# Performance work log

Measured on AMD Instinct MI355X. Metric: run time of the kernel, lower is better.

## Reference

```python
import jax, jax.numpy as jnp
import numpy as np

B, N, H = 32, 256, 1024
HEADS, NHID = 8, 128
NCLS = 7
BAND = 24
ALPHA = 0.2          # GAT leaky-relu slope
NEG = -9e15          # masked-attention fill, as in pyGAT


def setup_inputs() -> dict:
    key = jax.random.key(0)
    ks = jax.random.split(key, 16)
    def nrm(k, shp, s=0.02):
        return jax.random.normal(k, shp, dtype=jnp.float32) * s
    hidden_cls = jax.random.normal(ks[0], (B, N, H), dtype=jnp.float32)
    hidden_emo = jax.random.normal(ks[1], (B, N, H), dtype=jnp.float32)
    # causal band cliques, diagonal included (GAT uses clique - eye)
    t = jnp.arange(N)
    band = ((t[None, :] <= t[:, None]) & (t[None, :] > t[:, None] - BAND)).astype(jnp.float32)
    clique = jnp.broadcast_to(band, (B, N, N))
    labels = jax.random.randint(ks[2], (B, N), 0, NCLS)
    pooler_W = nrm(ks[3], (H, H)); pooler_b = jnp.zeros((H,), jnp.float32)
    gat_W = nrm(ks[4], (HEADS, H, NHID))
    gat_a1 = nrm(ks[5], (HEADS, NHID)); gat_a2 = nrm(ks[6], (HEADS, NHID))
    out_W = nrm(ks[7], (H, H))            # heads*nhid == H -> nclass=H
    out_a1 = nrm(ks[8], (H,)); out_a2 = nrm(ks[9], (H,))
    lin1_W = nrm(ks[10], (H, H)); lin1_b = jnp.zeros((H,), jnp.float32)
    lin0_W = nrm(ks[11], (2 * H, H)); lin0_b = jnp.zeros((H,), jnp.float32)
    cls_W = nrm(ks[12], (H, NCLS)); cls_b = jnp.zeros((NCLS,), jnp.float32)
    A = jax.random.uniform(ks[13], (NCLS, NCLS), dtype=jnp.float32) + 0.1
    hmm_A = A / A.sum(axis=1, keepdims=True)   # row-stochastic transition matrix
    return dict(hidden_cls=hidden_cls, hidden_emo=hidden_emo, clique=clique,
                labels=labels, pooler_W=pooler_W, pooler_b=pooler_b,
                gat_W=gat_W, gat_a1=gat_a1, gat_a2=gat_a2,
                out_W=out_W, out_a1=out_a1, out_a2=out_a2,
                lin1_W=lin1_W, lin1_b=lin1_b, lin0_W=lin0_W, lin0_b=lin0_b,
                cls_W=cls_W, cls_b=cls_b, hmm_A=hmm_A)


def _lrelu(x):
    return jnp.where(x > 0, x, ALPHA * x)


def reference(hidden_cls, hidden_emo, clique, labels, pooler_W, pooler_b,
              gat_W, gat_a1, gat_a2, out_W, out_a1, out_a2,
              lin1_W, lin1_b, lin0_W, lin0_b, cls_W, cls_b, hmm_A):
    # PoolerAll: dense + tanh on all token states (dropout = identity in eval)
    fea_cls = jnp.tanh(hidden_cls @ pooler_W + pooler_b)   # [B,N,H] (CLS per utt)
    fea_emo = jnp.tanh(hidden_emo @ pooler_W + pooler_b)   # [B,N,H] (mask tok per utt)

    eyeN = jnp.eye(N, dtype=clique.dtype)
    adjm = (clique - eyeN) > 0                             # [B,N,N] GAT adjacency

    def gat_one(x, am):                                    # x [N,H], am [N,N]
        Wh = jnp.einsum('nf,hfd->hnd', x, gat_W)           # [heads,N,nhid]
        e = _lrelu(jnp.einsum('hnd,hd->hn', Wh, gat_a1)[:, :, None]
                   + jnp.einsum('hnd,hd->hn', Wh, gat_a2)[:, None, :])
        att = jax.nn.softmax(jnp.where(am[None], e, NEG), axis=-1)
        h1 = jax.nn.elu(jnp.einsum('hnm,hmd->hnd', att, Wh))
        h1 = jnp.transpose(h1, (1, 0, 2)).reshape(N, HEADS * NHID)
        Wh2 = h1 @ out_W                                   # out attention layer (concat=False)
        e2 = _lrelu((Wh2 @ out_a1)[:, None] + (Wh2 @ out_a2)[None, :])
        h2 = jax.nn.softmax(jnp.where(am, e2, NEG), axis=-1) @ Wh2
        return jax.nn.elu(h2)                              # [N,H]

    gat_out = jax.vmap(gat_one)(fea_cls, adjm)             # [B,N,H]
    # row 0 replaced by (dropout of) fea_cls row 0, as in the original
    g = jnp.concatenate([fea_cls[:, :1], gat_out[:, 1:]], axis=1)
    g = jnp.concatenate([fea_cls, g @ lin1_W + lin1_b], axis=-1) @ lin0_W + lin0_b
    log_gat = jax.nn.softmax(g @ cls_W + cls_b, axis=-1)   # [B,N,NCLS] (probs)

    # HMM emission probs hmm_B(fea) = softmax(classifier(fea))
    Bprob = jax.nn.softmax(fea_emo @ cls_W + cls_b, axis=-1)  # [B,N,NCLS]
    P0 = jnp.full((NCLS,), 1.0 / NCLS, dtype=jnp.float32)
    AT = hmm_A.T

    def hmm_row(Bp, mrow):                                 # Bp [N,NCLS], mrow [N]
        def step(carry, xs):
            p, started = carry
            bt, m = xs
            p_init = P0 * bt; p_init = p_init / p_init.sum()
            p_tr = (AT @ p) * bt; p_tr = p_tr / p_tr.sum()
            p_new = jnp.where(started, p_tr, p_init)
            valid = m > 0.5
            return (jnp.where(valid, p_new, p), started | valid), None
        (p, _), _ = jax.lax.scan(step, (P0, jnp.asarray(False)), (Bp, mrow))
        return p                                           # final filtered posterior

    log_hmm = jax.vmap(lambda Bp, M: jax.vmap(lambda mr: hmm_row(Bp, mr))(M))(Bprob, clique)

    logits = jnp.log((log_gat + log_hmm) * 0.5).reshape(B * N, NCLS)
    lab = labels.reshape(B * N)
    mask = lab >= 0
    picked = jnp.take_along_axis(logits, jnp.where(mask, lab, 0)[:, None], axis=1)[:, 0]
    loss = -(jnp.where(mask, picked, 0.0).sum() / jnp.maximum(mask.sum(), 1).astype(jnp.float32))
    return loss, logits
```

## Files before the change

### kernel.cpp

```cpp
#include <hip/hip_runtime.h>
#include <hip/hip_bf16.h>
#include <math.h>

typedef __hip_bfloat16 bf16;
typedef __attribute__((ext_vector_type(8))) short short8;
typedef __attribute__((ext_vector_type(4))) float float4v;

static constexpr int Bb = 32, Nn = 256, Hh = 1024, HEADS = 8, NHID = 128, NCLS = 7, BAND = 24;
static constexpr int M = Bb * Nn;
static constexpr float ALPHA = 0.2f;
static constexpr long INEL = (long)M * Hh;

__device__ __forceinline__ float tof(bf16 x) { return __bfloat162float(x); }
__device__ __forceinline__ bf16 tob(float x) { return __float2bfloat16(x); }
__device__ __forceinline__ unsigned short f2bits(float x) {
    bf16 h = __float2bfloat16(x);
    return *(unsigned short*)&h;
}
__device__ __forceinline__ float bits2f(unsigned short u) {
    unsigned v = ((unsigned)u) << 16;
    float f;
    __builtin_memcpy(&f, &v, 4);
    return f;
}

__device__ __forceinline__ void gload16(const void* g, void* l) {
    __builtin_amdgcn_global_load_lds(
        (const __attribute__((address_space(1))) void*)g,
        (__attribute__((address_space(3))) void*)l, 16, 0, 0);
}

static constexpr long OFF_PWT  = 0;
static constexpr long OFF_PB   = 1048576;
static constexpr long OFF_WCT  = 1049600;
static constexpr long OFF_GA1  = 2098176;
static constexpr long OFF_GA2  = 2099200;
static constexpr long OFF_OWT  = 2100224;
static constexpr long OFF_OA1  = 3148800;
static constexpr long OFF_OA2  = 3149824;
static constexpr long OFF_L1WT = 3150848;
static constexpr long OFF_L1B  = 4199424;
static constexpr long OFF_L0WT = 4200448;
static constexpr long OFF_L0B  = 6297600;
static constexpr long OFF_CWT  = 6298624;
static constexpr long OFF_CB   = 6305792;
static constexpr long OFF_HA   = 6305799;
static constexpr long W_TOTAL  = 6305848;

__global__ void probe_k(const void* __restrict__ p, int* __restrict__ flag) {
    int t = threadIdx.x;
    int bad = 0;
    for (int i = t; i < 4096; i += 256) {
        float v = tof(((const bf16*)p)[i]);
        if (!(fabsf(v) < 1e4f)) bad = 1;
    }
    __shared__ int sb[256];
    sb[t] = bad; __syncthreads();
    for (int s = 128; s; s >>= 1) { if (t < s) sb[t] |= sb[t + s]; __syncthreads(); }
    if (t == 0) *flag = sb[0] ? 0 : 1;
}

__device__ __forceinline__ float ldany(const void* p, long i, int isb) {
    return isb ? tof(((const bf16*)p)[i]) : ((const float*)p)[i];
}

__global__ void convert_k(const int* __restrict__ flagp,
                          const void* pW, const void* pb, const void* gW,
                          const void* ga1, const void* ga2, const void* oW,
                          const void* oa1, const void* oa2, const void* l1W,
                          const void* l1b, const void* l0W, const void* l0b,
                          const void* cW, const void* cb, const void* hA,
                          bf16* __restrict__ dst) {
    long idx = (long)blockIdx.x * 256 + threadIdx.x;
    if (idx >= W_TOTAL) return;
    int isb = *flagp;
    const void* src; long si;
    if      (idx < OFF_PB)   { long l = idx;            long n = l >> 10, k = l & 1023;
                               src = pW;  si = k * 1024 + n; }
    else if (idx < OFF_WCT)  { src = pb;  si = idx - OFF_PB; }
    else if (idx < OFF_GA1)  { long l = idx - OFF_WCT;  long n = l >> 10, f = l & 1023;
                               long h = n >> 7, d = n & 127;
                               src = gW;  si = h * 131072 + f * 128 + d; }
    else if (idx < OFF_GA2)  { src = ga1; si = idx - OFF_GA1; }
    else if (idx < OFF_OWT)  { src = ga2; si = idx - OFF_GA2; }
    else if (idx < OFF_OA1)  { long l = idx - OFF_OWT;  long n = l >> 10, k = l & 1023;
                               src = oW;  si = k * 1024 + n; }
    else if (idx < OFF_OA2)  { src = oa1; si = idx - OFF_OA1; }
    else if (idx < OFF_L1WT) { src = oa2; si = idx - OFF_OA2; }
    else if (idx < OFF_L1B)  { long l = idx - OFF_L1WT; long n = l >> 10, k = l & 1023;
                               src = l1W; si = k * 1024 + n; }
    else if (idx < OFF_L0WT) { src = l1b; si = idx - OFF_L1B; }
    else if (idx < OFF_L0B)  { long l = idx - OFF_L0WT; long n = l >> 11, k = l & 2047;
                               src = l0W; si = k * 1024 + n; }
    else if (idx < OFF_CWT)  { src = l0b; si = idx - OFF_L0B; }
    else if (idx < OFF_CB)   { long l = idx - OFF_CWT;  long c = l >> 10, k = l & 1023;
                               src = cW;  si = k * 7 + c; }
    else if (idx < OFF_HA)   { src = cb;  si = idx - OFF_CB; }
    else                     { src = hA;  si = idx - OFF_HA; }
    dst[idx] = tob(ldany(src, si, isb));
}

__global__ void convin_k(const int* __restrict__ flagp, const void* __restrict__ s0,
                         const void* __restrict__ s1, bf16* __restrict__ d0,
                         bf16* __restrict__ d1) {
    const int isb = *flagp;
    long i = ((long)blockIdx.x * 256 + threadIdx.x) * 8;
    const void* s; bf16* d; long off;
    if (i < INEL) { s = s0; d = d0; off = i; }
    else          { s = s1; d = d1; off = i - INEL; }
    if (isb) {
        *(int4*)(d + off) = *(const int4*)((const bf16*)s + off);
    } else {
        const float* f = (const float*)s + off;
        unsigned short tmp[8];
        #pragma unroll
        for (int q = 0; q < 8; ++q) tmp[q] = f2bits(f[q]);
        *(int4*)(d + off) = *(int4*)tmp;
    }
}

template <int ACT>
__device__ __forceinline__ void gemm_core(const bf16* __restrict__ A,
                                          const bf16* __restrict__ Bt,
                                          const bf16* __restrict__ bias,
                                          bf16* __restrict__ Cout,
                                          unsigned short* As, unsigned short* Bs,
                                          int Nc, int K, int bm, int bn) {
    const int tid = threadIdx.x;
    const int lane = tid & 63;
    const int wave = tid >> 6;
    const int wm = (wave >> 1) * 64, wn = (wave & 1) * 64;
    const int l15 = lane & 15, quad = lane >> 4;
    const int r0 = wave * 32;
    const int lrow = lane >> 2, q = lane & 3;
    const int rA = r0 + lrow, rB = r0 + 16 + lrow;
    const int qa = (q ^ (rA & 3) ^ ((rA >> 2) & 3)) * 8;
    const int qb = (q ^ (rB & 3) ^ ((rB >> 2) & 3)) * 8;
    const int sc8 = (quad ^ (l15 & 3) ^ (l15 >> 2)) * 8;

    float4v acc[4][4];
    #pragma unroll
    for (int i = 0; i < 4; ++i)
        #pragma unroll
        for (int j = 0; j < 4; ++j) acc[i][j] = (float4v){0.f, 0.f, 0.f, 0.f};

    const bf16* ga0 = A + (long)(bm + rA) * K + qa;
    const bf16* ga1 = A + (long)(bm + rB) * K + qb;
    const bf16* gb0 = Bt + (long)(bn + rA) * K + qa;
    const bf16* gb1 = Bt + (long)(bn + rB) * K + qb;

    for (int k0 = 0; k0 < K; k0 += 64) {
        gload16(ga0 + k0,      As + r0 * 32);
        gload16(ga1 + k0,      As + (r0 + 16) * 32);
        gload16(ga0 + k0 + 32, As + 4096 + r0 * 32);
        gload16(ga1 + k0 + 32, As + 4096 + (r0 + 16) * 32);
        gload16(gb0 + k0,      Bs + r0 * 32);
        gload16(gb1 + k0,      Bs + (r0 + 16) * 32);
        gload16(gb0 + k0 + 32, Bs + 4096 + r0 * 32);
        gload16(gb1 + k0 + 32, Bs + 4096 + (r0 + 16) * 32);
        __syncthreads();
        #pragma unroll
        for (int ks = 0; ks < 2; ++ks) {
            const unsigned short* Au = As + ks * 4096;
            const unsigned short* Bu = Bs + ks * 4096;
            short8 af[4], bfr[4];
            #pragma unroll
            for (int i = 0; i < 4; ++i)
                af[i] = *(const short8*)(Au + (wm + i * 16 + l15) * 32 + sc8);
            #pragma unroll
            for (int j = 0; j < 4; ++j)
                bfr[j] = *(const short8*)(Bu + (wn + j * 16 + l15) * 32 + sc8);
            #pragma unroll
            for (int i = 0; i < 4; ++i)
                #pragma unroll
                for (int j = 0; j < 4; ++j)
                    acc[i][j] = __builtin_amdgcn_mfma_f32_16x16x32_bf16(af[i], bfr[j], acc[i][j], 0, 0, 0);
        }
        __syncthreads();
    }
    #pragma unroll
    for (int j = 0; j < 4; ++j) {
        int gn = bn + wn + j * 16 + l15;
        float bj = bias ? tof(bias[gn]) : 0.f;
        #pragma unroll
        for (int i = 0; i < 4; ++i) {
            #pragma unroll
            for (int r = 0; r < 4; ++r) {
                int gm = bm + wm + i * 16 + quad * 4 + r;
                float v = acc[i][j][r] + bj;
                if (ACT == 1) v = tanhf(v);
                Cout[(long)gm * Nc + gn] = tob(v);
            }
        }
    }
}

template <int ACT>
__global__ __launch_bounds__(256) void gemm_fast_k(const bf16* __restrict__ A,
                                                   const bf16* __restrict__ Bt,
                                                   const bf16* __restrict__ bias,
                                                   bf16* __restrict__ Cout,
                                                   int Nc, int K) {
    __shared__ unsigned short As[2 * 128 * 32];
    __shared__ unsigned short Bs[2 * 128 * 32];
    gemm_core<ACT>(A, Bt, bias, Cout, As, Bs, Nc, K, blockIdx.x * 128, blockIdx.y * 128);
}

__global__ __launch_bounds__(256) void gemmP_k(const bf16* __restrict__ A0,
                                               const bf16* __restrict__ A1,
                                               const bf16* __restrict__ Bt,
                                               const bf16* __restrict__ bias,
                                               bf16* __restrict__ C0,
                                               bf16* __restrict__ C1) {
    __shared__ unsigned short As[2 * 128 * 32];
    __shared__ unsigned short Bs[2 * 128 * 32];
    const bf16* A = blockIdx.z ? A1 : A0;
    bf16* C = blockIdx.z ? C1 : C0;
    gemm_core<1>(A, Bt, bias, C, As, Bs, Hh, Hh, blockIdx.x * 128, blockIdx.y * 128);
}

__global__ __launch_bounds__(256) void gemm2_fast_k(const bf16* __restrict__ A1,
                                                    const bf16* __restrict__ A2,
                                                    const bf16* __restrict__ Bt,
                                                    const bf16* __restrict__ bias,
                                                    bf16* __restrict__ Cout) {
    constexpr int Nc = 1024, K = 2048;
    __shared__ unsigned short As[2 * 128 * 32];
    __shared__ unsigned short Bs[2 * 128 * 32];
    const int tid = threadIdx.x;
    const int lane = tid & 63;
    const int wave = tid >> 6;
    const int wm = (wave >> 1) * 64, wn = (wave & 1) * 64;
    const int l15 = lane & 15, quad = lane >> 4;
    const int r0 = wave * 32;
    const int lrow = lane >> 2, q = lane & 3;
    const int rA = r0 + lrow, rB = r0 + 16 + lrow;
    const int qa = (q ^ (rA & 3) ^ ((rA >> 2) & 3)) * 8;
    const int qb = (q ^ (rB & 3) ^ ((rB >> 2) & 3)) * 8;
    const int sc8 = (quad ^ (l15 & 3) ^ (l15 >> 2)) * 8;
    const int bm = blockIdx.x * 128, bn = blockIdx.y * 128;

    float4v acc[4][4];
    #pragma unroll
    for (int i = 0; i < 4; ++i)
        #pragma unroll
        for (int j = 0; j < 4; ++j) acc[i][j] = (float4v){0.f, 0.f, 0.f, 0.f};

    const bf16* gb0 = Bt + (long)(bn + rA) * K + qa;
    const bf16* gb1 = Bt + (long)(bn + rB) * K + qb;
    for (int k0 = 0; k0 < K; k0 += 64) {
        const bf16* Asrc = (k0 < 1024) ? A1 : A2;
        int kl = k0 & 1023;
        const bf16* ga0 = Asrc + (long)(bm + rA) * 1024 + kl + qa;
        const bf16* ga1 = Asrc + (long)(bm + rB) * 1024 + kl + qb;
        gload16(ga0,      As + r0 * 32);
        gload16(ga1,      As + (r0 + 16) * 32);
        gload16(ga0 + 32, As + 4096 + r0 * 32);
        gload16(ga1 + 32, As + 4096 + (r0 + 16) * 32);
        gload16(gb0 + k0,      Bs + r0 * 32);
        gload16(gb1 + k0,      Bs + (r0 + 16) * 32);
        gload16(gb0 + k0 + 32, Bs + 4096 + r0 * 32);
        gload16(gb1 + k0 + 32, Bs + 4096 + (r0 + 16) * 32);
        __syncthreads();
        #pragma unroll
        for (int ks = 0; ks < 2; ++ks) {
            const unsigned short* Au = As + ks * 4096;
            const unsigned short* Bu = Bs + ks * 4096;
            short8 af[4], bfr[4];
            #pragma unroll
            for (int i = 0; i < 4; ++i)
                af[i] = *(const short8*)(Au + (wm + i * 16 + l15) * 32 + sc8);
            #pragma unroll
            for (int j = 0; j < 4; ++j)
                bfr[j] = *(const short8*)(Bu + (wn + j * 16 + l15) * 32 + sc8);
            #pragma unroll
            for (int i = 0; i < 4; ++i)
                #pragma unroll
                for (int j = 0; j < 4; ++j)
                    acc[i][j] = __builtin_amdgcn_mfma_f32_16x16x32_bf16(af[i], bfr[j], acc[i][j], 0, 0, 0);
        }
        __syncthreads();
    }
    #pragma unroll
    for (int j = 0; j < 4; ++j) {
        int gn = bn + wn + j * 16 + l15;
        float bj = tof(bias[gn]);
        #pragma unroll
        for (int i = 0; i < 4; ++i)
            #pragma unroll
            for (int r = 0; r < 4; ++r) {
                int gm = bm + wm + i * 16 + quad * 4 + r;
                Cout[(long)gm * Nc + gn] = tob(acc[i][j][r] + bj);
            }
    }
}

__global__ __launch_bounds__(256) void att1f_k(const bf16* __restrict__ Wh,
                                               const bf16* __restrict__ ga1,
                                               const bf16* __restrict__ ga2,
                                               bf16* __restrict__ h1) {
    __shared__ unsigned short S[152][128];
    __shared__ float f1s[152], f2s[152];
    __shared__ float att[128][25];
    const int bx = blockIdx.x;
    const int b = bx >> 4, h = (bx >> 1) & 7, half = bx & 1;
    const int nbase = half * 128;
    const int mstart = half ? (nbase - (BAND - 1)) : 0;
    const int mcount = half ? (256 - mstart) : 128;
    const int t = threadIdx.x;
    const int c = t & 15;

    float av1[8], av2[8];
    {
        union { int4 v; unsigned short us[8]; } u1, u2;
        u1.v = *(const int4*)(ga1 + h * 128 + c * 8);
        u2.v = *(const int4*)(ga2 + h * 128 + c * 8);
        #pragma unroll
        for (int qq = 0; qq < 8; ++qq) { av1[qq] = bits2f(u1.us[qq]); av2[qq] = bits2f(u2.us[qq]); }
    }

    const int iters = (mcount * 16 + 255) >> 8;
    for (int i = 0; i < iters; ++i) {
        int li = i * 256 + t;
        int mr = li >> 4;
        if (mr < mcount) {
            long ga = (long)(b * 256 + mstart + mr) * 1024 + h * 128 + c * 8;
            union { int4 v; unsigned short us[8]; } u;
            u.v = *(const int4*)(Wh + ga);
            float p1 = 0.f, p2 = 0.f;
            #pragma unroll
            for (int qq = 0; qq < 8; ++qq) {
                float f = bits2f(u.us[qq]);
                p1 += f * av1[qq]; p2 += f * av2[qq];
            }
            *(int4*)&S[mr][c * 8] = u.v;
            #pragma unroll
            for (int mask = 1; mask < 16; mask <<= 1) {
                p1 += __shfl_xor(p1, mask);
                p2 += __shfl_xor(p2, mask);
            }
            if (c == 0) { f1s[mr] = p1; f2s[mr] = p2; }
        }
    }
    __syncthreads();

    if (t < 128) {
        int n = nbase + t;
        if (n > 0) {
            int cnt = n < (BAND - 1) ? n : (BAND - 1);
            int m0 = n - cnt;
            float f1n = f1s[n - mstart];
            float e[BAND - 1];
            float mx = -1e30f;
            for (int i = 0; i < cnt; ++i) {
                float v = f1n + f2s[m0 + i - mstart];
                v = v > 0.f ? v : ALPHA * v;
                e[i] = v; mx = fmaxf(mx, v);
            }
            float ss = 0.f;
            for (int i = 0; i < cnt; ++i) { e[i] = __expf(e[i] - mx); ss += e[i]; }
            float inv = 1.0f / ss;
            for (int i = 0; i < cnt; ++i) att[t][i] = e[i] * inv;
        }
    }
    __syncthreads();

    const int wave = t >> 6, lane = t & 63;
    for (int ln = wave; ln < 128; ln += 4) {
        int n = nbase + ln;
        if (n == 0) continue;
        int cnt = n < (BAND - 1) ? n : (BAND - 1);
        int mr0 = n - cnt - mstart;
        float s0 = 0.f, s1 = 0.f;
        for (int i = 0; i < cnt; ++i) {
            float a = att[ln][i];
            unsigned u = *(const unsigned*)&S[mr0 + i][lane * 2];
            s0 += a * bits2f((unsigned short)(u & 0xffff));
            s1 += a * bits2f((unsigned short)(u >> 16));
        }
        s0 = s0 > 0.f ? s0 : expm1f(s0);
        s1 = s1 > 0.f ? s1 : expm1f(s1);
        unsigned out = (unsigned)f2bits(s0) | ((unsigned)f2bits(s1) << 16);
        *(unsigned*)(h1 + (long)(b * 256 + n) * 1024 + h * 128 + lane * 2) = out;
    }
}

__global__ void mean1_k(const bf16* __restrict__ Wh, bf16* __restrict__ h1) {
    int bh = blockIdx.x;
    int h = bh & 7, b = bh >> 3;
    int lane = threadIdx.x;
    float s0 = 0.f, s1 = 0.f;
    long base = (long)(b * 256) * 1024 + h * 128 + lane * 2;
    for (int m = 0; m < 256; ++m) {
        unsigned u = *(const unsigned*)(Wh + base + (long)m * 1024);
        s0 += bits2f((unsigned short)(u & 0xffff));
        s1 += bits2f((unsigned short)(u >> 16));
    }
    s0 *= (1.0f / 256.0f); s1 *= (1.0f / 256.0f);
    s0 = s0 > 0.f ? s0 : expm1f(s0);
    s1 = s1 > 0.f ? s1 : expm1f(s1);
    unsigned out = (unsigned)f2bits(s0) | ((unsigned)f2bits(s1) << 16);
    *(unsigned*)(h1 + base) = out;
}

__global__ void f12b_k(const bf16* __restrict__ Wh2, const bf16* __restrict__ a1,
                       const bf16* __restrict__ a2, float* __restrict__ f1b,
                       float* __restrict__ f2b) {
    int idx = blockIdx.x;
    int lane = threadIdx.x;
    const bf16* row = Wh2 + (long)idx * 1024 + lane * 16;
    float s1 = 0.f, s2 = 0.f;
    #pragma unroll
    for (int half = 0; half < 2; ++half) {
        union { int4 v; unsigned short us[8]; } x, w1, w2;
        x.v  = *(const int4*)(row + half * 8);
        w1.v = *(const int4*)(a1 + lane * 16 + half * 8);
        w2.v = *(const int4*)(a2 + lane * 16 + half * 8);
        #pragma unroll
        for (int q = 0; q < 8; ++q) {
            float f = bits2f(x.us[q]);
            s1 += f * bits2f(w1.us[q]);
            s2 += f * bits2f(w2.us[q]);
        }
    }
    #pragma unroll
    for (int off = 32; off; off >>= 1) {
        s1 += __shfl_down(s1, off);
        s2 += __shfl_down(s2, off);
    }
    if (lane == 0) { f1b[idx] = s1; f2b[idx] = s2; }
}

__global__ __launch_bounds__(256) void att2f_k(const bf16* __restrict__ Wh2,
                                               const float* __restrict__ f1b,
                                               const float* __restrict__ f2b,
                                               bf16* __restrict__ g) {
    __shared__ unsigned short S[152][128];
    __shared__ float att[128][25];
    const int bx = blockIdx.x;
    const int b = bx >> 4, half = (bx >> 3) & 1, jt = bx & 7;
    const int nbase = half * 128;
    const int mstart = half ? (nbase - (BAND - 1)) : 0;
    const int mcount = half ? (256 - mstart) : 128;
    const int t = threadIdx.x;
    const int c = t & 15;

    const int iters = (mcount * 16 + 255) >> 8;
    for (int i = 0; i < iters; ++i) {
        int li = i * 256 + t;
        int mr = li >> 4;
        if (mr < mcount) {
            long ga = (long)(b * 256 + mstart + mr) * 1024 + jt * 128 + c * 8;
            *(int4*)&S[mr][c * 8] = *(const int4*)(Wh2 + ga);
        }
    }
    __syncthreads();

    if (t < 128) {
        int n = nbase + t;
        if (n > 0) {
            int cnt = n < (BAND - 1) ? n : (BAND - 1);
            int m0 = n - cnt;
            float f1n = f1b[b * 256 + n];
            float e[BAND - 1];
            float mx = -1e30f;
            for (int i = 0; i < cnt; ++i) {
                float v = f1n + f2b[b * 256 + m0 + i];
                v = v > 0.f ? v : ALPHA * v;
                e[i] = v; mx = fmaxf(mx, v);
            }
            float ss = 0.f;
            for (int i = 0; i < cnt; ++i) { e[i] = __expf(e[i] - mx); ss += e[i]; }
            float inv = 1.0f / ss;
            for (int i = 0; i < cnt; ++i) att[t][i] = e[i] * inv;
        }
    }
    __syncthreads();

    const int wave = t >> 6, lane = t & 63;
    for (int ln = wave; ln < 128; ln += 4) {
        int n = nbase + ln;
        if (n == 0) continue;
        int cnt = n < (BAND - 1) ? n : (BAND - 1);
        int mr0 = n - cnt - mstart;
        float s0 = 0.f, s1 = 0.f;
        for (int i = 0; i < cnt; ++i) {
            float a = att[ln][i];
            unsigned u = *(const unsigned*)&S[mr0 + i][lane * 2];
            s0 += a * bits2f((unsigned short)(u & 0xffff));
            s1 += a * bits2f((unsigned short)(u >> 16));
        }
        s0 = s0 > 0.f ? s0 : expm1f(s0);
        s1 = s1 > 0.f ? s1 : expm1f(s1);
        unsigned out = (unsigned)f2bits(s0) | ((unsigned)f2bits(s1) << 16);
        *(unsigned*)(g + (long)(b * 256 + n) * 1024 + jt * 128 + lane * 2) = out;
    }
}

__global__ void g_row0_k(const bf16* __restrict__ fea_cls, bf16* __restrict__ g) {
    int b = blockIdx.x;
    int t = threadIdx.x;
    long base = (long)(b * 256) * 1024 + t * 8;
    *(int4*)(g + base) = *(const int4*)(fea_cls + base);
}

__global__ void cls7_k(const bf16* __restrict__ X, const bf16* __restrict__ Wt,
                       const bf16* __restrict__ b, float* __restrict__ out, int K) {
    int row = blockIdx.x;
    int lane = threadIdx.x;
    float xv[16];
    {
        const bf16* x = X + (long)row * K + lane * 16;
        union { int4 v; unsigned short us[8]; } u0, u1;
        u0.v = *(const int4*)x; u1.v = *(const int4*)(x + 8);
        #pragma unroll
        for (int q = 0; q < 8; ++q) { xv[q] = bits2f(u0.us[q]); xv[q + 8] = bits2f(u1.us[q]); }
    }
    float acc[NCLS];
    #pragma unroll
    for (int cc = 0; cc < NCLS; ++cc) {
        const bf16* wr = Wt + (long)cc * K + lane * 16;
        union { int4 v; unsigned short us[8]; } w0, w1;
        w0.v = *(const int4*)wr; w1.v = *(const int4*)(wr + 8);
        float s = 0.f;
        #pragma unroll
        for (int q = 0; q < 8; ++q) {
            s += xv[q] * bits2f(w0.us[q]);
            s += xv[q + 8] * bits2f(w1.us[q]);
        }
        acc[cc] = s;
    }
    #pragma unroll
    for (int cc = 0; cc < NCLS; ++cc)
        #pragma unroll
        for (int off = 32; off; off >>= 1) acc[cc] += __shfl_down(acc[cc], off);
    if (lane == 0) {
        float mx = -1e30f;
        #pragma unroll
        for (int cc = 0; cc < NCLS; ++cc) { acc[cc] += tof(b[cc]); mx = fmaxf(mx, acc[cc]); }
        float s = 0.f;
        #pragma unroll
        for (int cc = 0; cc < NCLS; ++cc) { acc[cc] = expf(acc[cc] - mx); s += acc[cc]; }
        float inv = 1.0f / s;
        #pragma unroll
        for (int cc = 0; cc < NCLS; ++cc) out[(long)row * NCLS + cc] = acc[cc] * inv;
    }
}

__global__ void hmm_k(const float* __restrict__ Bprob, const bf16* __restrict__ hmm_A,
                      float* __restrict__ out) {
    __shared__ float AT[NCLS][NCLS];
    int t = threadIdx.x;
    if (t < NCLS * NCLS) {
        int i = t / NCLS, j = t % NCLS;
        AT[i][j] = tof(hmm_A[j * NCLS + i]);
    }
    __syncthreads();
    int idx = blockIdx.x * blockDim.x + t;
    int n = idx & 255, b = idx >> 8;
    int t0 = n - (BAND - 1) > 0 ? n - (BAND - 1) : 0;
    const float* Bp = Bprob + (long)(b * 256) * NCLS;
    float p[NCLS];
    float s = 0.f;
    #pragma unroll
    for (int cc = 0; cc < NCLS; ++cc) { p[cc] = Bp[t0 * NCLS + cc]; s += p[cc]; }
    float inv = 1.0f / s;
    #pragma unroll
    for (int cc = 0; cc < NCLS; ++cc) p[cc] *= inv;
    for (int tt = t0 + 1; tt <= n; ++tt) {
        float q[NCLS]; float ss = 0.f;
        #pragma unroll
        for (int i = 0; i < NCLS; ++i) {
            float a = 0.f;
            #pragma unroll
            for (int j = 0; j < NCLS; ++j) a += AT[i][j] * p[j];
            a *= Bp[tt * NCLS + i];
            q[i] = a; ss += a;
        }
        float iv = 1.0f / ss;
        #pragma unroll
        for (int i = 0; i < NCLS; ++i) p[i] = q[i] * iv;
    }
    #pragma unroll
    for (int cc = 0; cc < NCLS; ++cc) out[(long)idx * NCLS + cc] = p[cc];
}

__global__ void zero_k(float* p) { *p = 0.f; }

__global__ void final_k(const float* __restrict__ lg, const float* __restrict__ lh,
                        const int* __restrict__ labels, void* __restrict__ out,
                        float* __restrict__ loss_acc, const int* __restrict__ flagp) {
    int idx = blockIdx.x * blockDim.x + threadIdx.x;
    const int isb = *flagp;
    float lo[NCLS];
    int lab = labels[idx];
    #pragma unroll
    for (int c = 0; c < NCLS; ++c) {
        float v = logf(0.5f * (lg[(long)idx * NCLS + c] + lh[(long)idx * NCLS + c]));
        lo[c] = v;
        long o = 1 + (long)idx * NCLS + c;
        if (isb) ((bf16*)out)[o] = tob(v);
        else     ((float*)out)[o] = v;
    }
    float picked = lo[lab];
    __shared__ float red[256];
    red[threadIdx.x] = picked;
    __syncthreads();
    for (int s = 128; s; s >>= 1) {
        if (threadIdx.x < s) red[threadIdx.x] += red[threadIdx.x + s];
        __syncthreads();
    }
    if (threadIdx.x == 0) atomicAdd(loss_acc, red[0]);
}

__global__ void loss_k(const float* __restrict__ acc, void* __restrict__ out,
                       const int* __restrict__ flagp) {
    float v = -acc[0] / (float)(Bb * Nn);
    if (*flagp) ((bf16*)out)[0] = tob(v);
    else        ((float*)out)[0] = v;
}

extern "C" void kernel_launch(void* const* d_in, const int* in_sizes, int n_in,
                              void* d_out, int out_size, void* d_ws, size_t ws_size,
                              hipStream_t stream) {
    const void* hidden_cls = d_in[0];
    const void* hidden_emo = d_in[1];
    const int* labels = (const int*)d_in[3];

    char* w = (char*)d_ws;
    bf16* C  = (bf16*)w;
    bf16* E  = C + INEL;
    bf16* Wb = E + INEL;
    bf16* H2 = Wb + INEL;
    bf16* wc = H2 + INEL;
    float* f1b   = (float*)(wc + W_TOTAL);
    float* f2b   = f1b + M;
    float* Bprob = f2b + M;
    float* lgat  = Bprob + (long)M * NCLS;
    float* lhmm  = lgat + (long)M * NCLS;
    float* loss_acc = lhmm + (long)M * NCLS;
    int*   flag  = (int*)(loss_acc + 1);

    dim3 gblk(256);
    dim3 ggrid(M / 128, Hh / 128);
    dim3 pgrid(M / 128, Hh / 128, 2);

    probe_k<<<1, 256, 0, stream>>>(d_in[4], flag);
    convert_k<<<(int)((W_TOTAL + 255) / 256), 256, 0, stream>>>(
        flag, d_in[4], d_in[5], d_in[6], d_in[7], d_in[8], d_in[9], d_in[10],
        d_in[11], d_in[12], d_in[13], d_in[14], d_in[15], d_in[16], d_in[17],
        d_in[18], wc);
    convin_k<<<(int)(2 * INEL / (256 * 8)), 256, 0, stream>>>(flag, hidden_emo, hidden_cls, Wb, H2);

    gemmP_k<<<pgrid, gblk, 0, stream>>>(Wb, H2, wc + OFF_PWT, wc + OFF_PB, E, C);
    cls7_k<<<M, 64, 0, stream>>>(E, wc + OFF_CWT, wc + OFF_CB, Bprob, Hh);
    gemm_fast_k<0><<<ggrid, gblk, 0, stream>>>(C, wc + OFF_WCT, (const bf16*)nullptr, Wb, Hh, Hh);
    att1f_k<<<512, 256, 0, stream>>>(Wb, wc + OFF_GA1, wc + OFF_GA2, E);
    mean1_k<<<Bb * HEADS, 64, 0, stream>>>(Wb, E);
    gemm_fast_k<0><<<ggrid, gblk, 0, stream>>>(E, wc + OFF_OWT, (const bf16*)nullptr, Wb, Hh, Hh);
    f12b_k<<<M, 64, 0, stream>>>(Wb, wc + OFF_OA1, wc + OFF_OA2, f1b, f2b);
    g_row0_k<<<Bb, 128, 0, stream>>>(C, E);
    att2f_k<<<512, 256, 0, stream>>>(Wb, f1b, f2b, E);
    gemm_fast_k<0><<<ggrid, gblk, 0, stream>>>(E, wc + OFF_L1WT, wc + OFF_L1B, Wb, Hh, Hh);
    gemm2_fast_k<<<ggrid, gblk, 0, stream>>>(C, Wb, wc + OFF_L0WT, wc + OFF_L0B, E);
    cls7_k<<<M, 64, 0, stream>>>(E, wc + OFF_CWT, wc + OFF_CB, lgat, Hh);
    hmm_k<<<M / 256, 256, 0, stream>>>(Bprob, wc + OFF_HA, lhmm);
    zero_k<<<1, 1, 0, stream>>>(loss_acc);
    final_k<<<M / 256, 256, 0, stream>>>(lgat, lhmm, labels, d_out, loss_acc, flag);
    loss_k<<<1, 1, 0, stream>>>(loss_acc, d_out, flag);
}
```

Measured before the change: 488.5 us.

## Fold lin1 GEMM into lin0 weights and fuse small kernels

Removes the separate lin1 GEMM over activations. The lin0 second-half weights are pre-multiplied with lin1_W inside the pooler GEMM launch (extra z-slice), and the folded bias is computed once in a small kernel. Conversion of weights and inputs is merged into one launch. The row-0 copy is folded into att2f, and the HMM filter is folded into the final loss kernel. This saves a full M×H×H GEMM and several launches, at the cost of an extra bf16 rounding of the combined weight product.

```diff
diff --git a/kernel.cpp b/kernel.cpp
--- a/kernel.cpp
+++ b/kernel.cpp
@@ -45,7 +45,9 @@
 static constexpr long OFF_CWT  = 6298624;
 static constexpr long OFF_CB   = 6305792;
 static constexpr long OFF_HA   = 6305799;
-static constexpr long W_TOTAL  = 6305848;
+static constexpr long OFF_L1WN = 6305848;
+static constexpr long W_TOTAL  = 7354424;
+static constexpr long CONV_TOTAL = W_TOTAL + (2 * INEL) / 8;
 
 __global__ void probe_k(const void* __restrict__ p, int* __restrict__ flag) {
     int t = threadIdx.x;
@@ -64,16 +66,34 @@
     return isb ? tof(((const bf16*)p)[i]) : ((const float*)p)[i];
 }
 
-__global__ void convert_k(const int* __restrict__ flagp,
+__global__ void convall_k(const int* __restrict__ flagp,
                           const void* pW, const void* pb, const void* gW,
                           const void* ga1, const void* ga2, const void* oW,
                           const void* oa1, const void* oa2, const void* l1W,
                           const void* l1b, const void* l0W, const void* l0b,
                           const void* cW, const void* cb, const void* hA,
-                          bf16* __restrict__ dst) {
+                          const void* in0, const void* in1,
+                          bf16* __restrict__ dst, bf16* __restrict__ din0,
+                          bf16* __restrict__ din1) {
     long idx = (long)blockIdx.x * 256 + threadIdx.x;
-    if (idx >= W_TOTAL) return;
+    if (idx >= CONV_TOTAL) return;
     int isb = *flagp;
+    if (idx >= W_TOTAL) {
+        long g = (idx - W_TOTAL) * 8;
+        const void* s; bf16* d; long off;
+        if (g < INEL) { s = in0; d = din0; off = g; }
+        else          { s = in1; d = din1; off = g - INEL; }
+        if (isb) {
+            *(int4*)(d + off) = *(const int4*)((const bf16*)s + off);
+        } else {
+            const float* f = (const float*)s + off;
+            unsigned short tmp[8];
+            #pragma unroll
+            for (int q = 0; q < 8; ++q) tmp[q] = f2bits(f[q]);
+            *(int4*)(d + off) = *(int4*)tmp;
+        }
+        return;
+    }
     const void* src; long si;
     if      (idx < OFF_PB)   { long l = idx;            long n = l >> 10, k = l & 1023;
                                src = pW;  si = k * 1024 + n; }
@@ -96,36 +116,29 @@
     else if (idx < OFF_CB)   { long l = idx - OFF_CWT;  long c = l >> 10, k = l & 1023;
                                src = cW;  si = k * 7 + c; }
     else if (idx < OFF_HA)   { src = cb;  si = idx - OFF_CB; }
-    else                     { src = hA;  si = idx - OFF_HA; }
+    else if (idx < OFF_L1WN) { src = hA;  si = idx - OFF_HA; }
+    else                     { src = l1W; si = idx - OFF_L1WN; }
     dst[idx] = tob(ldany(src, si, isb));
 }
 
-__global__ void convin_k(const int* __restrict__ flagp, const void* __restrict__ s0,
-                         const void* __restrict__ s1, bf16* __restrict__ d0,
-                         bf16* __restrict__ d1) {
-    const int isb = *flagp;
-    long i = ((long)blockIdx.x * 256 + threadIdx.x) * 8;
-    const void* s; bf16* d; long off;
-    if (i < INEL) { s = s0; d = d0; off = i; }
-    else          { s = s1; d = d1; off = i - INEL; }
-    if (isb) {
-        *(int4*)(d + off) = *(const int4*)((const bf16*)s + off);
-    } else {
-        const float* f = (const float*)s + off;
-        unsigned short tmp[8];
-        #pragma unroll
-        for (int q = 0; q < 8; ++q) tmp[q] = f2bits(f[q]);
-        *(int4*)(d + off) = *(int4*)tmp;
-    }
-}
-
-template <int ACT>
-__device__ __forceinline__ void gemm_core(const bf16* __restrict__ A,
-                                          const bf16* __restrict__ Bt,
+__global__ void bias2_k(const bf16* __restrict__ wc, bf16* __restrict__ b2) {
+    int n = blockIdx.x;
+    int lane = threadIdx.x;
+    const bf16* row = wc + OFF_L0WT + (long)n * 2048 + 1024;
+    const bf16* l1b = wc + OFF_L1B;
+    float s = 0.f;
+    for (int j = lane; j < 1024; j += 64) s += tof(l1b[j]) * tof(row[j]);
+    #pragma unroll
+    for (int off = 32; off; off >>= 1) s += __shfl_down(s, off);
+    if (lane == 0) b2[n] = tob(s + tof(wc[OFF_L0B + n]));
+}
+
+__device__ __forceinline__ void gemm_core(const bf16* __restrict__ A, int lda,
+                                          const bf16* __restrict__ Bt, int ldb,
                                           const bf16* __restrict__ bias,
                                           bf16* __restrict__ Cout,
                                           unsigned short* As, unsigned short* Bs,
-                                          int Nc, int K, int bm, int bn) {
+                                          int Nc, int K, int bm, int bn, int act) {
     const int tid = threadIdx.x;
     const int lane = tid & 63;
     const int wave = tid >> 6;
@@ -144,10 +157,10 @@
         #pragma unroll
         for (int j = 0; j < 4; ++j) acc[i][j] = (float4v){0.f, 0.f, 0.f, 0.f};
 
-    const bf16* ga0 = A + (long)(bm + rA) * K + qa;
-    const bf16* ga1 = A + (long)(bm + rB) * K + qb;
-    const bf16* gb0 = Bt + (long)(bn + rA) * K + qa;
-    const bf16* gb1 = Bt + (long)(bn + rB) * K + qb;
+    const bf16* ga0 = A + (long)(bm + rA) * lda + qa;
+    const bf16* ga1 = A + (long)(bm + rB) * lda + qb;
+    const bf16* gb0 = Bt + (long)(bn + rA) * ldb + qa;
+    const bf16* gb1 = Bt + (long)(bn + rB) * ldb + qb;
 
     for (int k0 = 0; k0 < K; k0 += 64) {
         gload16(ga0 + k0,      As + r0 * 32);
@@ -188,14 +201,13 @@
             for (int r = 0; r < 4; ++r) {
                 int gm = bm + wm + i * 16 + quad * 4 + r;
                 float v = acc[i][j][r] + bj;
-                if (ACT == 1) v = tanhf(v);
+                if (act == 1) v = tanhf(v);
                 Cout[(long)gm * Nc + gn] = tob(v);
             }
         }
     }
 }
 
-template <int ACT>
 __global__ __launch_bounds__(256) void gemm_fast_k(const bf16* __restrict__ A,
                                                    const bf16* __restrict__ Bt,
                                                    const bf16* __restrict__ bias,
@@ -203,7 +215,7 @@
                                                    int Nc, int K) {
     __shared__ unsigned short As[2 * 128 * 32];
     __shared__ unsigned short Bs[2 * 128 * 32];
-    gemm_core<ACT>(A, Bt, bias, Cout, As, Bs, Nc, K, blockIdx.x * 128, blockIdx.y * 128);
+    gemm_core(A, K, Bt, K, bias, Cout, As, Bs, Nc, K, blockIdx.x * 128, blockIdx.y * 128, 0);
 }
 
 __global__ __launch_bounds__(256) void gemmP_k(const bf16* __restrict__ A0,
@@ -211,20 +223,30 @@
                                                const bf16* __restrict__ Bt,
                                                const bf16* __restrict__ bias,
                                                bf16* __restrict__ C0,
-                                               bf16* __restrict__ C1) {
+                                               bf16* __restrict__ C1,
+                                               const bf16* __restrict__ wgA,
+                                               const bf16* __restrict__ wgB,
+                                               bf16* __restrict__ wgC) {
     __shared__ unsigned short As[2 * 128 * 32];
     __shared__ unsigned short Bs[2 * 128 * 32];
-    const bf16* A = blockIdx.z ? A1 : A0;
-    bf16* C = blockIdx.z ? C1 : C0;
-    gemm_core<1>(A, Bt, bias, C, As, Bs, Hh, Hh, blockIdx.x * 128, blockIdx.y * 128);
+    const int z = blockIdx.z;
+    if (z == 2) {
+        if (blockIdx.x >= 8) return;
+        gemm_core(wgA, 2048, wgB, 1024, (const bf16*)nullptr, wgC, As, Bs,
+                  1024, 1024, blockIdx.x * 128, blockIdx.y * 128, 0);
+    } else {
+        gemm_core(z ? A1 : A0, 1024, Bt, 1024, bias, z ? C1 : C0, As, Bs,
+                  1024, 1024, blockIdx.x * 128, blockIdx.y * 128, 1);
+    }
 }
 
 __global__ __launch_bounds__(256) void gemm2_fast_k(const bf16* __restrict__ A1,
+                                                    const bf16* __restrict__ B1,
                                                     const bf16* __restrict__ A2,
-                                                    const bf16* __restrict__ Bt,
+                                                    const bf16* __restrict__ B2,
                                                     const bf16* __restrict__ bias,
                                                     bf16* __restrict__ Cout) {
-    constexpr int Nc = 1024, K = 2048;
+    constexpr int Nc = 1024;
     __shared__ unsigned short As[2 * 128 * 32];
     __shared__ unsigned short Bs[2 * 128 * 32];
     const int tid = threadIdx.x;
@@ -246,21 +268,24 @@
         #pragma unroll
         for (int j = 0; j < 4; ++j) acc[i][j] = (float4v){0.f, 0.f, 0.f, 0.f};
 
-    const bf16* gb0 = Bt + (long)(bn + rA) * K + qa;
-    const bf16* gb1 = Bt + (long)(bn + rB) * K + qb;
-    for (int k0 = 0; k0 < K; k0 += 64) {
-        const bf16* Asrc = (k0 < 1024) ? A1 : A2;
-        int kl = k0 & 1023;
+    for (int k0 = 0; k0 < 2048; k0 += 64) {
+        const int sel = (k0 < 1024);
+        const bf16* Asrc = sel ? A1 : A2;
+        const bf16* Bsrc = sel ? B1 : B2;
+        const int ldb = sel ? 2048 : 1024;
+        const int kl = k0 & 1023;
         const bf16* ga0 = Asrc + (long)(bm + rA) * 1024 + kl + qa;
         const bf16* ga1 = Asrc + (long)(bm + rB) * 1024 + kl + qb;
+        const bf16* gb0 = Bsrc + (long)(bn + rA) * ldb + kl + qa;
+        const bf16* gb1 = Bsrc + (long)(bn + rB) * ldb + kl + qb;
         gload16(ga0,      As + r0 * 32);
         gload16(ga1,      As + (r0 + 16) * 32);
         gload16(ga0 + 32, As + 4096 + r0 * 32);
         gload16(ga1 + 32, As + 4096 + (r0 + 16) * 32);
-        gload16(gb0 + k0,      Bs + r0 * 32);
-        gload16(gb1 + k0,      Bs + (r0 + 16) * 32);
-        gload16(gb0 + k0 + 32, Bs + 4096 + r0 * 32);
-        gload16(gb1 + k0 + 32, Bs + 4096 + (r0 + 16) * 32);
+        gload16(gb0,      Bs + r0 * 32);
+        gload16(gb1,      Bs + (r0 + 16) * 32);
+        gload16(gb0 + 32, Bs + 4096 + r0 * 32);
+        gload16(gb1 + 32, Bs + 4096 + (r0 + 16) * 32);
         __syncthreads();
         #pragma unroll
         for (int ks = 0; ks < 2; ++ks) {
@@ -434,6 +459,7 @@
 __global__ __launch_bounds__(256) void att2f_k(const bf16* __restrict__ Wh2,
                                                const float* __restrict__ f1b,
                                                const float* __restrict__ f2b,
+                                               const bf16* __restrict__ fea_cls,
                                                bf16* __restrict__ g) {
     __shared__ unsigned short S[152][128];
     __shared__ float att[128][25];
@@ -444,6 +470,11 @@
     const int mcount = half ? (256 - mstart) : 128;
     const int t = threadIdx.x;
     const int c = t & 15;
+
+    if (half == 0 && t < 16) {
+        long base = (long)(b * 256) * 1024 + jt * 128 + t * 8;
+        *(int4*)(g + base) = *(const int4*)(fea_cls + base);
+    }
 
     const int iters = (mcount * 16 + 255) >> 8;
     for (int i = 0; i < iters; ++i) {
@@ -497,13 +528,6 @@
     }
 }
 
-__global__ void g_row0_k(const bf16* __restrict__ fea_cls, bf16* __restrict__ g) {
-    int b = blockIdx.x;
-    int t = threadIdx.x;
-    long base = (long)(b * 256) * 1024 + t * 8;
-    *(int4*)(g + base) = *(const int4*)(fea_cls + base);
-}
-
 __global__ void cls7_k(const bf16* __restrict__ X, const bf16* __restrict__ Wt,
                        const bf16* __restrict__ b, float* __restrict__ out, int K) {
     int row = blockIdx.x;
@@ -547,56 +571,49 @@
     }
 }
 
-__global__ void hmm_k(const float* __restrict__ Bprob, const bf16* __restrict__ hmm_A,
-                      float* __restrict__ out) {
+__global__ void zero_k(float* p) { *p = 0.f; }
+
+__global__ void final_k(const float* __restrict__ lg, const float* __restrict__ Bprob,
+                        const bf16* __restrict__ hmm_A, const int* __restrict__ labels,
+                        void* __restrict__ out, float* __restrict__ loss_acc,
+                        const int* __restrict__ flagp) {
     __shared__ float AT[NCLS][NCLS];
     int t = threadIdx.x;
-    if (t < NCLS * NCLS) {
-        int i = t / NCLS, j = t % NCLS;
-        AT[i][j] = tof(hmm_A[j * NCLS + i]);
-    }
+    if (t < NCLS * NCLS) AT[t / NCLS][t % NCLS] = tof(hmm_A[(t % NCLS) * NCLS + t / NCLS]);
     __syncthreads();
-    int idx = blockIdx.x * blockDim.x + t;
+    int idx = blockIdx.x * 256 + t;
     int n = idx & 255, b = idx >> 8;
     int t0 = n - (BAND - 1) > 0 ? n - (BAND - 1) : 0;
     const float* Bp = Bprob + (long)(b * 256) * NCLS;
     float p[NCLS];
-    float s = 0.f;
-    #pragma unroll
-    for (int cc = 0; cc < NCLS; ++cc) { p[cc] = Bp[t0 * NCLS + cc]; s += p[cc]; }
-    float inv = 1.0f / s;
-    #pragma unroll
-    for (int cc = 0; cc < NCLS; ++cc) p[cc] *= inv;
-    for (int tt = t0 + 1; tt <= n; ++tt) {
-        float q[NCLS]; float ss = 0.f;
-        #pragma unroll
-        for (int i = 0; i < NCLS; ++i) {
-            float a = 0.f;
-            #pragma unroll
-            for (int j = 0; j < NCLS; ++j) a += AT[i][j] * p[j];
-            a *= Bp[tt * NCLS + i];
-            q[i] = a; ss += a;
-        }
-        float iv = 1.0f / ss;
-        #pragma unroll
-        for (int i = 0; i < NCLS; ++i) p[i] = q[i] * iv;
-    }
-    #pragma unroll
-    for (int cc = 0; cc < NCLS; ++cc) out[(long)idx * NCLS + cc] = p[cc];
-}
-
-__global__ void zero_k(float* p) { *p = 0.f; }
-
-__global__ void final_k(const float* __restrict__ lg, const float* __restrict__ lh,
-                        const int* __restrict__ labels, void* __restrict__ out,
-                        float* __restrict__ loss_acc, const int* __restrict__ flagp) {
-    int idx = blockIdx.x * blockDim.x + threadIdx.x;
+    {
+        float s = 0.f;
+        #pragma unroll
+        for (int cc = 0; cc < NCLS; ++cc) { p[cc] = Bp[t0 * NCLS + cc]; s += p[cc]; }
+        float inv = 1.0f / s;
+        #pragma unroll
+        for (int cc = 0; cc < NCLS; ++cc) p[cc] *= inv;
+        for (int tt = t0 + 1; tt <= n; ++tt) {
+            float qv[NCLS]; float ss = 0.f;
+            #pragma unroll
+            for (int i = 0; i < NCLS; ++i) {
+                float a = 0.f;
+                #pragma unroll
+                for (int j = 0; j < NCLS; ++j) a += AT[i][j] * p[j];
+                a *= Bp[tt * NCLS + i];
+                qv[i] = a; ss += a;
+            }
+            float iv = 1.0f / ss;
+            #pragma unroll
+            for (int i = 0; i < NCLS; ++i) p[i] = qv[i] * iv;
+        }
+    }
     const int isb = *flagp;
+    int lab = labels[idx];
     float lo[NCLS];
-    int lab = labels[idx];
     #pragma unroll
     for (int c = 0; c < NCLS; ++c) {
-        float v = logf(0.5f * (lg[(long)idx * NCLS + c] + lh[(long)idx * NCLS + c]));
+        float v = logf(0.5f * (lg[(long)idx * NCLS + c] + p[c]));
         lo[c] = v;
         long o = 1 + (long)idx * NCLS + c;
         if (isb) ((bf16*)out)[o] = tob(v);
@@ -604,13 +621,13 @@
     }
     float picked = lo[lab];
     __shared__ float red[256];
-    red[threadIdx.x] = picked;
+    red[t] = picked;
     __syncthreads();
     for (int s = 128; s; s >>= 1) {
-        if (threadIdx.x < s) red[threadIdx.x] += red[threadIdx.x + s];
+        if (t < s) red[t] += red[t + s];
         __syncthreads();
     }
-    if (threadIdx.x == 0) atomicAdd(loss_acc, red[0]);
+    if (t == 0) atomicAdd(loss_acc, red[0]);
 }
 
 __global__ void loss_k(const float* __restrict__ acc, void* __restrict__ out,
@@ -633,39 +650,38 @@
     bf16* Wb = E + INEL;
     bf16* H2 = Wb + INEL;
     bf16* wc = H2 + INEL;
-    float* f1b   = (float*)(wc + W_TOTAL);
+    bf16* WgT = wc + W_TOTAL;
+    bf16* b2  = WgT + (long)Hh * Hh;
+    float* f1b   = (float*)(b2 + Hh);
     float* f2b   = f1b + M;
     float* Bprob = f2b + M;
     float* lgat  = Bprob + (long)M * NCLS;
-    float* lhmm  = lgat + (long)M * NCLS;
-    float* loss_acc = lhmm + (long)M * NCLS;
+    float* loss_acc = lgat + (long)M * NCLS;
     int*   flag  = (int*)(loss_acc + 1);
 
     dim3 gblk(256);
     dim3 ggrid(M / 128, Hh / 128);
-    dim3 pgrid(M / 128, Hh / 128, 2);
+    dim3 pgrid(M / 128, Hh / 128, 3);
 
     probe_k<<<1, 256, 0, stream>>>(d_in[4], flag);
-    convert_k<<<(int)((W_TOTAL + 255) / 256), 256, 0, stream>>>(
+    convall_k<<<(int)((CONV_TOTAL + 255) / 256), 256, 0, stream>>>(
         flag, d_in[4], d_in[5], d_in[6], d_in[7], d_in[8], d_in[9], d_in[10],
         d_in[11], d_in[12], d_in[13], d_in[14], d_in[15], d_in[16], d_in[17],
-        d_in[18], wc);
-    convin_k<<<(int)(2 * INEL / (256 * 8)), 256, 0, stream>>>(flag, hidden_emo, hidden_cls, Wb, H2);
-
-    gemmP_k<<<pgrid, gblk, 0, stream>>>(Wb, H2, wc + OFF_PWT, wc + OFF_PB, E, C);
+        d_in[18], hidden_emo, hidden_cls, wc, Wb, H2);
+    bias2_k<<<Hh, 64, 0, stream>>>(wc, b2);
+
+    gemmP_k<<<pgrid, gblk, 0, stream>>>(Wb, H2, wc + OFF_PWT, wc + OFF_PB, E, C,
+                                        wc + OFF_L0WT + 1024, wc + OFF_L1WN, WgT);
     cls7_k<<<M, 64, 0, stream>>>(E, wc + OFF_CWT, wc + OFF_CB, Bprob, Hh);
-    gemm_fast_k<0><<<ggrid, gblk, 0, stream>>>(C, wc + OFF_WCT, (const bf16*)nullptr, Wb, Hh, Hh);
+    gemm_fast_k<<<ggrid, gblk, 0, stream>>>(C, wc + OFF_WCT, (const bf16*)nullptr, Wb, Hh, Hh);
     att1f_k<<<512, 256, 0, stream>>>(Wb, wc + OFF_GA1, wc + OFF_GA2, E);
     mean1_k<<<Bb * HEADS, 64, 0, stream>>>(Wb, E);
-    gemm_fast_k<0><<<ggrid, gblk, 0, stream>>>(E, wc + OFF_OWT, (const bf16*)nullptr, Wb, Hh, Hh);
+    gemm_fast_k<<<ggrid, gblk, 0, stream>>>(E, wc + OFF_OWT, (const bf16*)nullptr, Wb, Hh, Hh);
     f12b_k<<<M, 64, 0, stream>>>(Wb, wc + OFF_OA1, wc + OFF_OA2, f1b, f2b);
-    g_row0_k<<<Bb, 128, 0, stream>>>(C, E);
-    att2f_k<<<512, 256, 0, stream>>>(Wb, f1b, f2b, E);
-    gemm_fast_k<0><<<ggrid, gblk, 0, stream>>>(E, wc + OFF_L1WT, wc + OFF_L1B, Wb, Hh, Hh);
-    gemm2_fast_k<<<ggrid, gblk, 0, stream>>>(C, Wb, wc + OFF_L0WT, wc + OFF_L0B, E);
-    cls7_k<<<M, 64, 0, stream>>>(E, wc + OFF_CWT, wc + OFF_CB, lgat, Hh);
-    hmm_k<<<M / 256, 256, 0, stream>>>(Bprob, wc + OFF_HA, lhmm);
+    att2f_k<<<512, 256, 0, stream>>>(Wb, f1b, f2b, C, E);
+    gemm2_fast_k<<<ggrid, gblk, 0, stream>>>(C, wc + OFF_L0WT, E, WgT, b2, Wb);
+    cls7_k<<<M, 64, 0, stream>>>(Wb, wc + OFF_CWT, wc + OFF_CB, lgat, Hh);
     zero_k<<<1, 1, 0, stream>>>(loss_acc);
-    final_k<<<M / 256, 256, 0, stream>>>(lgat, lhmm, labels, d_out, loss_acc, flag);
+    final_k<<<M / 256, 256, 0, stream>>>(lgat, Bprob, wc + OFF_HA, labels, d_out, loss_acc, flag);
     loss_k<<<1, 1, 0, stream>>>(loss_acc, d_out, flag);
 }
```

New measurement: 489.9 us. Within noise of the previous version (+0.3%).
